# Performance work log

Hardware: AMD Instinct MI355X
Metric: run time of the kernel (lower is better)

The kernel has to match this reference:

```python
import jax, jax.numpy as jnp
import numpy as np

B, F, S = 2, 512, 1024
E = 4
I = 1024          # intermediate = 2 * features
K = 3             # conv kernel size
INIT_SCALE = 1.0
EPS = 1e-5
SLOPE = 0.02


def setup_inputs() -> dict:
    key = jax.random.key(0)
    k = jax.random.split(key, 6)
    inp = jax.random.normal(k[0], (B, F, S), jnp.float32)
    divisor = (jnp.arange(S, dtype=jnp.float32) + 1.0).reshape(1, 1, S)
    w0_gate = jax.random.normal(k[1], (E, F, 1), jnp.float32) * (F ** -0.5)
    w0 = jax.random.normal(k[2], (E, F, 3 * I), jnp.float32) * (F ** -0.5)
    w1 = jax.random.normal(k[3], (3 * I, I, K), jnp.float32) * ((I * K) ** -0.5)
    w2_gate = jax.random.normal(k[4], (E, I, 1), jnp.float32) * (I ** -0.5)
    w2 = jax.random.normal(k[5], (E, I, F), jnp.float32) * (I ** -0.5)
    return {"inp": inp, "divisor": divisor, "w0_gate": w0_gate, "w0": w0,
            "w1": w1, "w2_gate": w2_gate, "w2": w2}


def _norm(x):
    # channel norm over dim 1: subtract mean, divide by scaled L2 norm
    x = x - jnp.mean(x, axis=1, keepdims=True)
    n = jnp.sqrt(jnp.sum(x * x, axis=1, keepdims=True)) * (x.shape[1] ** -0.5)
    return x / (n + EPS)


def _moe(x, gate, w):
    # x: [B,F,S]; gate: [E,F,1]; w: [E,F,D]
    logits = jnp.einsum('bfs,ef->bes', x, gate[:, :, 0])          # [B,E,S]
    gates = jax.nn.softmax(logits, axis=1)
    idx = jnp.argmax(logits, axis=1)                              # [B,S]
    one_hot = jax.nn.one_hot(idx, w.shape[0], dtype=x.dtype)      # [B,S,E]
    # straight-through gumbel-style gate: hard one-hot fwd, soft grad
    gumbel = jnp.transpose(one_hot, (0, 2, 1)) - jax.lax.stop_gradient(gates) + gates  # [B,E,S]
    xs = jnp.transpose(x, (0, 2, 1))                              # [B,S,F]
    out = jnp.zeros((x.shape[0], x.shape[2], w.shape[2]), x.dtype)
    for e in range(w.shape[0]):  # small fixed expert count
        mask = one_hot[:, :, e][:, :, None]                       # [B,S,1]
        out = out + mask * ((xs * gumbel[:, e, :, None]) @ w[e])
    loss = jnp.sum(jnp.mean(gates, axis=(0, 2)) * jnp.mean(one_hot, axis=(0, 1)))
    return loss, jnp.transpose(out, (0, 2, 1))                    # [B,D,S]


def _conv1d(x, w, causal_pad):
    if causal_pad and w.shape[-1] > 1:
        x = jnp.pad(x, ((0, 0), (0, 0), (w.shape[-1] - 1, 0)))
    return jax.lax.conv_general_dilated(
        x, w, window_strides=(1,), padding='VALID',
        dimension_numbers=('NCH', 'OIH', 'NCH'), feature_group_count=1)


def reference(inp, divisor, w0_gate, w0, w1, w2_gate, w2):
    loss0, h = _moe(inp, w0_gate, w0)                 # [B,3I,S]
    depth, scale, shift = jnp.split(h, 3, axis=1)     # each [B,I,S]
    cum = jnp.cumsum(depth, axis=-1)
    h = jax.nn.leaky_relu(_norm(cum / divisor * scale + shift), SLOPE)
    h = _conv1d(h, w1, causal_pad=True)               # [B,3I,S]
    s0, s1, sh = jnp.split(h, 3, axis=1)
    h = jax.nn.leaky_relu(_norm(s0 * s1 + sh), SLOPE)
    loss1, out = _moe(h, w2_gate, w2)                 # [B,F,S]
    return out * INIT_SCALE, loss0 + loss1
```

## Files before the change

### kernel.cpp

```cpp
#include <hip/hip_runtime.h>
#include <hip/hip_bf16.h>

#define SDIM 1024

typedef float f32x4 __attribute__((ext_vector_type(4)));
typedef short short8 __attribute__((ext_vector_type(8)));

__device__ __forceinline__ unsigned short f2bf(float f) {
    __hip_bfloat16 h = __float2bfloat16(f);
    return *reinterpret_cast<unsigned short*>(&h);
}
__device__ __forceinline__ float bf2f(unsigned short u) {
    return __uint_as_float(((unsigned int)u) << 16);
}
__device__ __forceinline__ void gload_lds16(const unsigned short* g, unsigned short* l) {
    __builtin_amdgcn_global_load_lds((const __attribute__((address_space(1))) void*)g,
                                     (__attribute__((address_space(3))) void*)l, 16, 0, 0);
}

__device__ __forceinline__ void tr_split(
    const float* __restrict__ in, unsigned short* __restrict__ oh,
    unsigned short* __restrict__ ol, int R, int C, size_t sliceStride,
    int bx, int by, int slice, int tid, float (*t)[33])
{
    int c0 = bx * 32, r0 = by * 32;
    int cc = tid & 31, r8 = tid >> 5;
    const float* ip = in + slice * sliceStride;
    #pragma unroll
    for (int k = 0; k < 4; ++k) {
        int r = r8 + k * 8;
        t[r][cc] = ip[(size_t)(r0 + r) * C + c0 + cc];
    }
    __syncthreads();
    #pragma unroll
    for (int k = 0; k < 4; ++k) {
        int rr = r8 + k * 8;
        float v = t[cc][rr];
        unsigned short hi = f2bf(v);
        unsigned short lo = f2bf(v - bf2f(hi));
        size_t o = slice * sliceStride + (size_t)(c0 + rr) * R + r0 + cc;
        oh[o] = hi; ol[o] = lo;
    }
}

__global__ __launch_bounds__(256) void prep_kernel(
    const float* __restrict__ inp, const float* __restrict__ w0,
    const float* __restrict__ w1,
    unsigned short* __restrict__ xTh, unsigned short* __restrict__ xTl,
    unsigned short* __restrict__ w0Th, unsigned short* __restrict__ w0Tl,
    unsigned short* __restrict__ w1Th, unsigned short* __restrict__ w1Tl,
    const float* __restrict__ wg, int* __restrict__ idx, float* __restrict__ acc)
{
    __shared__ float t[32][33];
    __shared__ float wgs[4 * 512];
    __shared__ float part[32][4][9];
    __shared__ float la[8];
    int id = blockIdx.x;
    int tid = threadIdx.x;
    if (id < 1024) {
        int bx = id & 31, by = (id >> 5) & 15, slice = id >> 9;
        tr_split(inp, xTh, xTl, 512, 1024, (size_t)512 * 1024, bx, by, slice, tid, t);
    } else if (id < 7168) {
        int m = id - 1024;
        int bx = m % 96, by = (m / 96) & 15, slice = m / 1536;
        tr_split(w0, w0Th, w0Tl, 512, 3072, (size_t)512 * 3072, bx, by, slice, tid, t);
    } else if (id < 19456) {
        int tt = (id - 7168) * 256 + tid;
        int o = tt >> 10, i = tt & 1023;
        const float* p = w1 + (size_t)o * 3072 + i * 3;
        #pragma unroll
        for (int k = 0; k < 3; ++k) {
            float v = p[k];
            unsigned short hi = f2bf(v);
            unsigned short lo = f2bf(v - bf2f(hi));
            size_t off = (size_t)k * 3145728 + (size_t)o * 1024 + i;
            w1Th[off] = hi; w1Tl[off] = lo;
        }
    } else {
        if (tid < 8) la[tid] = 0.f;
        for (int l = tid; l < 2048; l += 256) wgs[l] = wg[l];
        __syncthreads();
        int t0 = (id - 19456) * 8;
        int b = t0 >> 10, s0 = t0 & 1023;
        int sl = tid & 7, fg = tid >> 3;
        float l0 = 0.f, l1 = 0.f, l2 = 0.f, l3 = 0.f;
        for (int f = fg; f < 512; f += 32) {
            float xv = inp[((size_t)b * 512 + f) * SDIM + s0 + sl];
            l0 += xv * wgs[f];
            l1 += xv * wgs[512 + f];
            l2 += xv * wgs[1024 + f];
            l3 += xv * wgs[1536 + f];
        }
        part[fg][0][sl] = l0; part[fg][1][sl] = l1;
        part[fg][2][sl] = l2; part[fg][3][sl] = l3;
        __syncthreads();
        for (int h = 16; h >= 1; h >>= 1) {
            if (fg < h) {
                #pragma unroll
                for (int e = 0; e < 4; ++e) part[fg][e][sl] += part[fg + h][e][sl];
            }
            __syncthreads();
        }
        if (fg == 0) {
            float L[4] = {part[0][0][sl], part[0][1][sl], part[0][2][sl], part[0][3][sl]};
            float m = fmaxf(fmaxf(L[0], L[1]), fmaxf(L[2], L[3]));
            float e0 = expf(L[0] - m), e1 = expf(L[1] - m), e2 = expf(L[2] - m), e3 = expf(L[3] - m);
            float inv = 1.0f / (e0 + e1 + e2 + e3);
            int best = 0; float bv = L[0];
            if (L[1] > bv) { bv = L[1]; best = 1; }
            if (L[2] > bv) { bv = L[2]; best = 2; }
            if (L[3] > bv) { bv = L[3]; best = 3; }
            idx[t0 + sl] = best;
            atomicAdd(&la[0], e0 * inv);
            atomicAdd(&la[1], e1 * inv);
            atomicAdd(&la[2], e2 * inv);
            atomicAdd(&la[3], e3 * inv);
            atomicAdd(&la[4 + best], 1.0f);
        }
        __syncthreads();
        if (tid < 8) atomicAdd(&acc[tid], la[tid]);
    }
}

__global__ __launch_bounds__(1024) void sort_kernel(
    const int* __restrict__ idx, int* __restrict__ perm, int* __restrict__ eSorted)
{
    int b = blockIdx.x;
    int tid = threadIdx.x;
    int lane = tid & 63, w = tid >> 6;
    int e = idx[(b << 10) + tid];
    __shared__ int wcnt[16][4];
    __shared__ int woff[16][4];
    int r = 0;
    unsigned long long lt = (1ull << lane) - 1ull;
    #pragma unroll
    for (int eo = 0; eo < 4; ++eo) {
        unsigned long long m = __ballot(e == eo);
        if (lane == 0) wcnt[w][eo] = __popcll(m);
        if (e == eo) r = __popcll(m & lt);
    }
    __syncthreads();
    if (tid == 0) {
        int baseAcc = 0;
        for (int eo = 0; eo < 4; ++eo)
            for (int ww = 0; ww < 16; ++ww) { woff[ww][eo] = baseAcc; baseAcc += wcnt[ww][eo]; }
    }
    __syncthreads();
    int pos = woff[w][e] + r;
    perm[(b << 10) + pos] = tid;
    eSorted[(b << 10) + pos] = e;
}

__global__ __launch_bounds__(768) void moe_split_kernel(
    const unsigned short* __restrict__ base, unsigned int XH, unsigned int XL,
    unsigned int WH, unsigned int WL,
    const int* __restrict__ perm, const int* __restrict__ eSorted,
    float* __restrict__ out)
{
    extern __shared__ unsigned short lds[];
    const int BUF = 40960;
    int id = blockIdx.x;
    int wg = (id & 7) * 32 + (id >> 3);
    int t0 = (wg & 7) * 256;
    int d0 = (wg >> 3) * 96;
    int b = t0 >> 10, s0 = t0 & 1023;
    int tid = threadIdx.x;
    int lane = tid & 63;
    int lm = lane & 15, q = lane >> 4;
    int wid = tid >> 6;
    int wm = (wid >> 2) * 32, wn = (wid & 3) * 64;

    int eLo = eSorted[(b << 10) + s0];
    int eHi = eSorted[(b << 10) + s0 + 255];

    unsigned int gofs[7];
    int lofs[7], doSeg[7];
    #pragma unroll
    for (int j = 0; j < 7; ++j) {
        int seg = wid + 12 * j;
        gofs[j] = 0; lofs[j] = 0; doSeg[j] = 0;
        if (seg < 80) {
            int row = seg * 16 + (lane >> 2);
            int slot = lane & 3;
            int c = slot ^ ((row >> 1) & 3);
            unsigned int src;
            int act = 1;
            if (row < 512) {
                int gr = (row < 256) ? row : row - 256;
                unsigned int hb = (row < 256) ? XH : XL;
                int tj = perm[(b << 10) + s0 + gr];
                src = hb + (unsigned int)(((b << 10) + tj) * 512) + c * 8;
            } else {
                int R = row - 512;
                unsigned int hb = WH;
                if (R >= 384) { R -= 384; hb = WL; }
                int e = R / 96, dl = R - e * 96;
                act = (e >= eLo && e <= eHi) ? 1 : 0;
                src = hb + (unsigned int)((e * 3072 + d0 + dl) * 512) + c * 8;
            }
            gofs[j] = src;
            lofs[j] = seg * 512 + lane * 8;
            doSeg[j] = act;
        }
    }

    int bofH[4];
    #pragma unroll
    for (int fn = 0; fn < 4; ++fn) {
        int row = wn + fn * 16 + lm;
        bofH[fn] = row * 32 + ((q ^ ((row >> 1) & 3)) << 3);
    }
    int aofH[4][2];
    #pragma unroll
    for (int e = 0; e < 4; ++e)
        #pragma unroll
        for (int fm = 0; fm < 2; ++fm) {
            int row = 512 + e * 96 + wm + fm * 16 + lm;
            aofH[e][fm] = row * 32 + ((q ^ ((row >> 1) & 3)) << 3);
        }

    int eidx[4], sv[4];
    #pragma unroll
    for (int fn = 0; fn < 4; ++fn) {
        int sl = (b << 10) + s0 + wn + fn * 16 + lm;
        eidx[fn] = eSorted[sl];
        sv[fn]   = perm[sl];
    }
    bool presF[4][4], presE[4];
    #pragma unroll
    for (int e = 0; e < 4; ++e) {
        presE[e] = false;
        #pragma unroll
        for (int fn = 0; fn < 4; ++fn) {
            presF[e][fn] = __any(eidx[fn] == e);
            presE[e] = presE[e] || presF[e][fn];
        }
    }

    f32x4 acc[2][4];
    #pragma unroll
    for (int fm = 0; fm < 2; ++fm)
        #pragma unroll
        for (int fn = 0; fn < 4; ++fn)
            acc[fm][fn] = (f32x4){0.f, 0.f, 0.f, 0.f};

    const short8 z = {0, 0, 0, 0, 0, 0, 0, 0};

    #pragma unroll
    for (int j = 0; j < 7; ++j)
        if (doSeg[j]) gload_lds16(base + gofs[j], lds + lofs[j]);

    int curOfs = 0;
    for (int f0 = 0; f0 < 512; f0 += 32) {
        __syncthreads();
        int nxtOfs = curOfs ^ BUF;
        if (f0 + 32 < 512) {
            #pragma unroll
            for (int j = 0; j < 7; ++j)
                if (doSeg[j]) gload_lds16(base + gofs[j] + f0 + 32, lds + nxtOfs + lofs[j]);
        }

        const unsigned short* lb = lds + curOfs;
        short8 bh[4], bl[4];
        #pragma unroll
        for (int fn = 0; fn < 4; ++fn) {
            bh[fn] = *(const short8*)(lb + bofH[fn]);
            bl[fn] = *(const short8*)(lb + bofH[fn] + 8192);
        }
        #pragma unroll
        for (int e = 0; e < 4; ++e) {
            if (presE[e]) {
                short8 ah[2], al[2];
                #pragma unroll
                for (int fm = 0; fm < 2; ++fm) {
                    ah[fm] = *(const short8*)(lb + aofH[e][fm]);
                    al[fm] = *(const short8*)(lb + aofH[e][fm] + 12288);
                }
                __builtin_amdgcn_s_setprio(1);
                #pragma unroll
                for (int fn = 0; fn < 4; ++fn) {
                    if (presF[e][fn]) {
                        short8 bmH = (eidx[fn] == e) ? bh[fn] : z;
                        short8 bmL = (eidx[fn] == e) ? bl[fn] : z;
                        #pragma unroll
                        for (int fm = 0; fm < 2; ++fm) {
                            acc[fm][fn] = __builtin_amdgcn_mfma_f32_16x16x32_bf16(ah[fm], bmH, acc[fm][fn], 0, 0, 0);
                            acc[fm][fn] = __builtin_amdgcn_mfma_f32_16x16x32_bf16(ah[fm], bmL, acc[fm][fn], 0, 0, 0);
                            acc[fm][fn] = __builtin_amdgcn_mfma_f32_16x16x32_bf16(al[fm], bmH, acc[fm][fn], 0, 0, 0);
                        }
                    }
                }
                __builtin_amdgcn_s_setprio(0);
            }
        }
        curOfs = nxtOfs;
    }

    #pragma unroll
    for (int fm = 0; fm < 2; ++fm)
        #pragma unroll
        for (int fn = 0; fn < 4; ++fn) {
            int d = d0 + wm + fm * 16 + q * 4;
            float* op = out + ((size_t)b * 3072 + d) * SDIM + sv[fn];
            #pragma unroll
            for (int r = 0; r < 4; ++r)
                op[(size_t)r * SDIM] = acc[fm][fn][r];
        }
}

__global__ __launch_bounds__(1024) void conv_split_kernel(
    const unsigned short* __restrict__ base, unsigned int GH, unsigned int GL,
    unsigned int WH, unsigned int WL, unsigned int ZB, float* __restrict__ h1T)
{
    extern __shared__ unsigned short lds[];
    const int BUF = 35328;
    int id = blockIdx.x;
    int wg = (id & 7) * 32 + (id >> 3);
    int t0 = (wg & 7) * 256;
    int o0 = (wg >> 3) * 96;
    int b = t0 >> 10, s0 = t0 & 1023;
    int tid = threadIdx.x;
    int lane = tid & 63;
    int lm = lane & 15, q = lane >> 4;
    int wid = tid >> 6;
    int wm = (wid >> 3) * 48, wn = (wid & 7) * 32;
    int krot = wid % 3;

    unsigned int gofs[5];
    int lofs[5];
    int nseg = (wid < 5) ? 5 : 4;
    #pragma unroll
    for (int j = 0; j < 5; ++j) {
        int seg = wid + 16 * j;
        gofs[j] = ZB; lofs[j] = 0;
        if (seg < 69) {
            int row = seg * 16 + (lane >> 2);
            int slot = lane & 3;
            int c = slot ^ ((row >> 1) & 3);
            unsigned int src;
            if (row < 528) {
                int gr = (row < 264) ? row : row - 264;
                unsigned int hb = (row < 264) ? GH : GL;
                int s = s0 - 2 + gr;
                if (s < 0) src = ZB + c * 8;
                else { if (s > 1023) s = 1023;
                       src = hb + ((unsigned int)((b << 10) + s) << 10) + c * 8; }
            } else {
                int R = row - 528;
                unsigned int hb = WH;
                if (R >= 288) { R -= 288; hb = WL; }
                int k = R / 96, ol = R - k * 96;
                src = hb + (unsigned int)k * 3145728u + ((unsigned int)(o0 + ol) << 10) + c * 8;
            }
            gofs[j] = src;
            lofs[j] = seg * 512 + lane * 8;
        }
    }

    int aofH[3][3], aofL[3][3], bofH[3][2], bofL[3][2];
    #pragma unroll
    for (int kk = 0; kk < 3; ++kk) {
        int k = kk + krot; if (k >= 3) k -= 3;
        #pragma unroll
        for (int fm = 0; fm < 3; ++fm) {
            int R = k * 96 + wm + fm * 16 + lm;
            int rh = 528 + R, rl = 816 + R;
            aofH[kk][fm] = rh * 32 + ((q ^ ((rh >> 1) & 3)) << 3);
            aofL[kk][fm] = rl * 32 + ((q ^ ((rl >> 1) & 3)) << 3);
        }
        #pragma unroll
        for (int fn = 0; fn < 2; ++fn) {
            int rh = wn + fn * 16 + lm + k;
            int rl = rh + 264;
            bofH[kk][fn] = rh * 32 + ((q ^ ((rh >> 1) & 3)) << 3);
            bofL[kk][fn] = rl * 32 + ((q ^ ((rl >> 1) & 3)) << 3);
        }
    }

    f32x4 acc[3][2];
    #pragma unroll
    for (int fm = 0; fm < 3; ++fm)
        #pragma unroll
        for (int fn = 0; fn < 2; ++fn)
            acc[fm][fn] = (f32x4){0.f, 0.f, 0.f, 0.f};

    #pragma unroll
    for (int j = 0; j < 5; ++j)
        if (j < nseg) gload_lds16(base + gofs[j], lds + lofs[j]);

    int curOfs = 0;
    for (int i0 = 0; i0 < 1024; i0 += 32) {
        __syncthreads();
        int nxtOfs = curOfs ^ BUF;
        if (i0 + 32 < 1024) {
            #pragma unroll
            for (int j = 0; j < 5; ++j)
                if (j < nseg) gload_lds16(base + gofs[j] + i0 + 32, lds + nxtOfs + lofs[j]);
        }

        const unsigned short* lb = lds + curOfs;
        #pragma unroll
        for (int kk = 0; kk < 3; ++kk) {
            short8 ah[3], al[3], bh[2], bl[2];
            #pragma unroll
            for (int fm = 0; fm < 3; ++fm) {
                ah[fm] = *(const short8*)(lb + aofH[kk][fm]);
                al[fm] = *(const short8*)(lb + aofL[kk][fm]);
            }
            #pragma unroll
            for (int fn = 0; fn < 2; ++fn) {
                bh[fn] = *(const short8*)(lb + bofH[kk][fn]);
                bl[fn] = *(const short8*)(lb + bofL[kk][fn]);
            }
            __builtin_amdgcn_s_setprio(1);
            #pragma unroll
            for (int fm = 0; fm < 3; ++fm)
                #pragma unroll
                for (int fn = 0; fn < 2; ++fn) {
                    acc[fm][fn] = __builtin_amdgcn_mfma_f32_16x16x32_bf16(ah[fm], bh[fn], acc[fm][fn], 0, 0, 0);
                    acc[fm][fn] = __builtin_amdgcn_mfma_f32_16x16x32_bf16(ah[fm], bl[fn], acc[fm][fn], 0, 0, 0);
                    acc[fm][fn] = __builtin_amdgcn_mfma_f32_16x16x32_bf16(al[fm], bh[fn], acc[fm][fn], 0, 0, 0);
                }
            __builtin_amdgcn_s_setprio(0);
        }
        curOfs = nxtOfs;
    }

    #pragma unroll
    for (int fm = 0; fm < 3; ++fm)
        #pragma unroll
        for (int fn = 0; fn < 2; ++fn) {
            int o = o0 + wm + fm * 16 + q * 4;
            int s = s0 + wn + fn * 16 + lm;
            *(f32x4*)(h1T + ((size_t)((b << 10) + s)) * 3072 + o) = acc[fm][fn];
        }
}

__global__ __launch_bounds__(256) void moe_kernel(
    const unsigned short* __restrict__ xT, const unsigned short* __restrict__ wT,
    const int* __restrict__ perm, const int* __restrict__ eSorted,
    float* __restrict__ out, int Fdim, int Ddim, const float* __restrict__ accv)
{
    if (blockIdx.x == 0 && threadIdx.x == 0) {
        float l = 0.f;
        #pragma unroll
        for (int e = 0; e < 4; ++e)
            l += accv[e] * accv[4 + e] + accv[8 + e] * accv[12 + e];
        out[2 * 512 * 1024] = l * (1.0f / (2048.0f * 2048.0f));
    }
    __shared__ unsigned short lds[384 * 32];
    int id = blockIdx.x;
    int chunk = gridDim.x >> 3;
    int wg = (id & 7) * chunk + (id >> 3);
    int t0 = (wg & 15) * 128;
    int d0 = (wg >> 4) * 64;
    int b = t0 >> 10, s0 = t0 & 1023;
    int tid = threadIdx.x;
    int lane = tid & 63, wid = tid >> 6;
    int lm = lane & 15, q = lane >> 4;
    int wm = (wid >> 1) * 32, wn = (wid & 1) * 64;

    int eLo = eSorted[(b << 10) + s0];
    int eHi = eSorted[(b << 10) + s0 + 127];

    const unsigned short* gsrc[6];
    int lofs[6], doSeg[6];
    #pragma unroll
    for (int j = 0; j < 6; ++j) {
        int seg = wid + 4 * j;
        int row = seg * 16 + (lane >> 2);
        int slot = lane & 3;
        int c = slot ^ ((row >> 1) & 3);
        int act = 1;
        const unsigned short* src;
        if (row < 128) {
            int tj = perm[(b << 10) + s0 + row];
            src = xT + (size_t)((b << 10) + tj) * Fdim + c * 8;
        } else {
            int R = row - 128;
            int e = R >> 6;
            act = (e >= eLo && e <= eHi) ? 1 : 0;
            src = wT + (size_t)(e * Ddim + d0 + (R & 63)) * Fdim + c * 8;
        }
        gsrc[j] = src; lofs[j] = seg * 512 + lane * 8; doSeg[j] = act;
    }

    int bof[4], aof[4][2];
    #pragma unroll
    for (int fn = 0; fn < 4; ++fn) {
        int row = wn + fn * 16 + lm;
        bof[fn] = row * 32 + ((q ^ ((row >> 1) & 3)) << 3);
    }
    #pragma unroll
    for (int e = 0; e < 4; ++e)
        #pragma unroll
        for (int fm = 0; fm < 2; ++fm) {
            int R = 128 + e * 64 + wm + fm * 16 + lm;
            aof[e][fm] = R * 32 + ((q ^ ((R >> 1) & 3)) << 3);
        }

    int eidx[4], sv[4];
    #pragma unroll
    for (int fn = 0; fn < 4; ++fn) {
        int sl = (b << 10) + s0 + wn + fn * 16 + lm;
        eidx[fn] = eSorted[sl];
        sv[fn]   = perm[sl];
    }
    bool presF[4][4], presE[4];
    #pragma unroll
    for (int e = 0; e < 4; ++e) {
        presE[e] = false;
        #pragma unroll
        for (int fn = 0; fn < 4; ++fn) {
            presF[e][fn] = __any(eidx[fn] == e);
            presE[e] = presE[e] || presF[e][fn];
        }
    }

    f32x4 acc[2][4];
    #pragma unroll
    for (int fm = 0; fm < 2; ++fm)
        #pragma unroll
        for (int fn = 0; fn < 4; ++fn)
            acc[fm][fn] = (f32x4){0.f, 0.f, 0.f, 0.f};

    const short8 z = {0, 0, 0, 0, 0, 0, 0, 0};

    for (int f0 = 0; f0 < Fdim; f0 += 32) {
        __syncthreads();
        #pragma unroll
        for (int j = 0; j < 6; ++j)
            if (doSeg[j]) gload_lds16(gsrc[j] + f0, lds + lofs[j]);
        __syncthreads();

        short8 bf[4];
        #pragma unroll
        for (int fn = 0; fn < 4; ++fn)
            bf[fn] = *(const short8*)(lds + bof[fn]);
        #pragma unroll
        for (int e = 0; e < 4; ++e) {
            if (presE[e]) {
                short8 af[2];
                #pragma unroll
                for (int fm = 0; fm < 2; ++fm)
                    af[fm] = *(const short8*)(lds + aof[e][fm]);
                #pragma unroll
                for (int fn = 0; fn < 4; ++fn) {
                    if (presF[e][fn]) {
                        short8 bm = (eidx[fn] == e) ? bf[fn] : z;
                        #pragma unroll
                        for (int fm = 0; fm < 2; ++fm)
                            acc[fm][fn] = __builtin_amdgcn_mfma_f32_16x16x32_bf16(af[fm], bm, acc[fm][fn], 0, 0, 0);
                    }
                }
            }
        }
    }

    #pragma unroll
    for (int fm = 0; fm < 2; ++fm)
        #pragma unroll
        for (int fn = 0; fn < 4; ++fn) {
            int d = d0 + wm + fm * 16 + q * 4;
            float* op = out + ((size_t)b * Ddim + d) * SDIM + sv[fn];
            #pragma unroll
            for (int r = 0; r < 4; ++r)
                op[(size_t)r * SDIM] = acc[fm][fn][r];
        }
}

__global__ __launch_bounds__(256) void cumsum_w2t_kernel(
    const float* __restrict__ h1, const float* __restrict__ divisor,
    float* __restrict__ y, const float* __restrict__ w2, unsigned short* __restrict__ w2T)
{
    __shared__ float tsh[32][33];
    __shared__ float wsum[4];
    int blk = blockIdx.x;
    int tid = threadIdx.x;
    if (blk >= 2048) {
        int m = blk - 2048;
        int bx = m & 15, by = (m >> 4) & 31, slice = m >> 9;
        int c0 = bx * 32, r0 = by * 32;
        int cc = tid & 31, r8 = tid >> 5;
        const float* ip = w2 + (size_t)slice * 524288;
        unsigned short* op = w2T + (size_t)slice * 524288;
        #pragma unroll
        for (int k = 0; k < 4; ++k) {
            int r = r8 + k * 8;
            tsh[r][cc] = ip[(size_t)(r0 + r) * 512 + c0 + cc];
        }
        __syncthreads();
        #pragma unroll
        for (int k = 0; k < 4; ++k) {
            int rr = r8 + k * 8;
            op[(size_t)(c0 + rr) * 1024 + r0 + cc] = f2bf(tsh[cc][rr]);
        }
        return;
    }
    int b = blk >> 10, i = blk & 1023;
    const float4* dp = (const float4*)(h1 + ((size_t)b * 3072 + i) * SDIM);
    const float4* sp = (const float4*)(h1 + ((size_t)b * 3072 + 1024 + i) * SDIM);
    const float4* hp = (const float4*)(h1 + ((size_t)b * 3072 + 2048 + i) * SDIM);
    float4 v = dp[tid];
    float c0 = v.x, c1 = c0 + v.y, c2 = c1 + v.z, c3 = c2 + v.w;
    int lane = tid & 63, w = tid >> 6;
    float sc = c3;
    #pragma unroll
    for (int off = 1; off < 64; off <<= 1) {
        float p = __shfl_up(sc, off);
        if (lane >= off) sc += p;
    }
    if (lane == 63) wsum[w] = sc;
    __syncthreads();
    float wbase = 0.f;
    #pragma unroll
    for (int ww = 0; ww < 4; ++ww)
        if (ww < w) wbase += wsum[ww];
    float base = wbase + sc - c3;
    float4 scv = sp[tid], sh = hp[tid];
    float4 dv = ((const float4*)divisor)[tid];
    float4 o;
    o.x = (base + c0) / dv.x * scv.x + sh.x;
    o.y = (base + c1) / dv.y * scv.y + sh.y;
    o.z = (base + c2) / dv.z * scv.z + sh.z;
    o.w = (base + c3) / dv.w * scv.w + sh.w;
    ((float4*)(y + ((size_t)b * 1024 + i) * SDIM))[tid] = o;
}

__global__ __launch_bounds__(256) void norm0_kernel(
    const float* __restrict__ g, unsigned short* __restrict__ oh,
    unsigned short* __restrict__ ol)
{
    int blk = blockIdx.x;
    int b = blk >> 7;
    int s0 = (blk & 127) * 8;
    int tid = threadIdx.x;
    int sg = tid & 7, grp = tid >> 3;
    int s = s0 + sg;
    const float* bp = g + ((size_t)b * 1024) * SDIM + s;
    float v[32];
    float sum = 0.f, ssq = 0.f;
    #pragma unroll
    for (int j = 0; j < 32; ++j) {
        float x = bp[(size_t)(grp * 32 + j) * SDIM];
        v[j] = x; sum += x; ssq += x * x;
    }
    __shared__ float rs[32][8], rq[32][8], stat[2][8];
    rs[grp][sg] = sum; rq[grp][sg] = ssq;
    __syncthreads();
    for (int h = 16; h >= 1; h >>= 1) {
        if (grp < h) { rs[grp][sg] += rs[grp + h][sg]; rq[grp][sg] += rq[grp + h][sg]; }
        __syncthreads();
    }
    if (grp == 0) {
        float S1 = rs[0][sg], S2 = rq[0][sg];
        float mean = S1 * (1.0f / 1024.0f);
        float ssc = fmaxf(S2 - 1024.0f * mean * mean, 0.0f);
        stat[0][sg] = mean;
        stat[1][sg] = 1.0f / (sqrtf(ssc) * (1.0f / 32.0f) + 1e-5f);
    }
    __syncthreads();
    float mean = stat[0][sg], inv = stat[1][sg];
    size_t tbase = (((size_t)b << 10) + s) * 1024 + grp * 32;
    #pragma unroll
    for (int j0 = 0; j0 < 32; j0 += 4) {
        unsigned short uh[4], ul[4];
        #pragma unroll
        for (int jj = 0; jj < 4; ++jj) {
            float o = (v[j0 + jj] - mean) * inv;
            o = (o >= 0.f) ? o : 0.02f * o;
            uh[jj] = f2bf(o);
            ul[jj] = f2bf(o - bf2f(uh[jj]));
        }
        *(ushort4*)(oh + tbase + j0) = (ushort4){uh[0], uh[1], uh[2], uh[3]};
        *(ushort4*)(ol + tbase + j0) = (ushort4){ul[0], ul[1], ul[2], ul[3]};
    }
}

__global__ __launch_bounds__(256) void normgate_kernel(
    const float* __restrict__ h1T, const float* __restrict__ wg,
    unsigned short* __restrict__ outT, int* __restrict__ idx, float* __restrict__ acc)
{
    int blk = blockIdx.x;
    int b = blk >> 7;
    int s0 = (blk & 127) * 8;
    int tid = threadIdx.x;
    int sg = tid & 7, grp = tid >> 3;
    int s = s0 + sg;
    const float* row = h1T + ((size_t)((b << 10) + s)) * 3072;
    float v[32];
    float sum = 0.f, ssq = 0.f;
    #pragma unroll
    for (int j0 = 0; j0 < 32; j0 += 4) {
        int i = grp * 32 + j0;
        float4 av = *(const float4*)(row + i);
        float4 mv = *(const float4*)(row + 1024 + i);
        float4 dv = *(const float4*)(row + 2048 + i);
        float x0 = av.x * mv.x + dv.x;
        float x1 = av.y * mv.y + dv.y;
        float x2 = av.z * mv.z + dv.z;
        float x3 = av.w * mv.w + dv.w;
        v[j0] = x0; v[j0 + 1] = x1; v[j0 + 2] = x2; v[j0 + 3] = x3;
        sum += x0 + x1 + x2 + x3;
        ssq += x0 * x0 + x1 * x1 + x2 * x2 + x3 * x3;
    }
    __shared__ float rs[32][8], rq[32][8], stat[2][8];
    rs[grp][sg] = sum; rq[grp][sg] = ssq;
    __syncthreads();
    for (int h = 16; h >= 1; h >>= 1) {
        if (grp < h) { rs[grp][sg] += rs[grp + h][sg]; rq[grp][sg] += rq[grp + h][sg]; }
        __syncthreads();
    }
    if (grp == 0) {
        float S1 = rs[0][sg], S2 = rq[0][sg];
        float mean = S1 * (1.0f / 1024.0f);
        float ssc = fmaxf(S2 - 1024.0f * mean * mean, 0.0f);
        stat[0][sg] = mean;
        stat[1][sg] = 1.0f / (sqrtf(ssc) * (1.0f / 32.0f) + 1e-5f);
    }
    __syncthreads();
    float mean = stat[0][sg], inv = stat[1][sg];
    float l0 = 0.f, l1 = 0.f, l2 = 0.f, l3 = 0.f;
    size_t tbase = (((size_t)b << 10) + s) * 1024 + grp * 32;
    #pragma unroll
    for (int j0 = 0; j0 < 32; j0 += 4) {
        unsigned short u[4];
        #pragma unroll
        for (int jj = 0; jj < 4; ++jj) {
            int i = grp * 32 + j0 + jj;
            float o = (v[j0 + jj] - mean) * inv;
            o = (o >= 0.f) ? o : 0.02f * o;
            u[jj] = f2bf(o);
            l0 += o * wg[i];
            l1 += o * wg[1024 + i];
            l2 += o * wg[2048 + i];
            l3 += o * wg[3072 + i];
        }
        *(ushort4*)(outT + tbase + j0) = (ushort4){u[0], u[1], u[2], u[3]};
    }
    __shared__ float pl[4][32][8];
    __shared__ float la[8];
    pl[0][grp][sg] = l0; pl[1][grp][sg] = l1;
    pl[2][grp][sg] = l2; pl[3][grp][sg] = l3;
    if (tid < 8) la[tid] = 0.f;
    __syncthreads();
    for (int h = 16; h >= 1; h >>= 1) {
        if (grp < h) {
            #pragma unroll
            for (int e = 0; e < 4; ++e) pl[e][grp][sg] += pl[e][grp + h][sg];
        }
        __syncthreads();
    }
    if (grp == 0) {
        float L[4] = {pl[0][0][sg], pl[1][0][sg], pl[2][0][sg], pl[3][0][sg]};
        float m = fmaxf(fmaxf(L[0], L[1]), fmaxf(L[2], L[3]));
        float e0 = expf(L[0] - m), e1 = expf(L[1] - m), e2 = expf(L[2] - m), e3 = expf(L[3] - m);
        float invs = 1.0f / (e0 + e1 + e2 + e3);
        int best = 0; float bv = L[0];
        if (L[1] > bv) { bv = L[1]; best = 1; }
        if (L[2] > bv) { bv = L[2]; best = 2; }
        if (L[3] > bv) { bv = L[3]; best = 3; }
        idx[(b << 10) + s] = best;
        atomicAdd(&la[0], e0 * invs);
        atomicAdd(&la[1], e1 * invs);
        atomicAdd(&la[2], e2 * invs);
        atomicAdd(&la[3], e3 * invs);
        atomicAdd(&la[4 + best], 1.0f);
    }
    __syncthreads();
    if (tid < 8) atomicAdd(&acc[8 + tid], la[tid]);
}

extern "C" void kernel_launch(void* const* d_in, const int* in_sizes, int n_in,
                              void* d_out, int out_size, void* d_ws, size_t ws_size,
                              hipStream_t stream) {
    const float* inp     = (const float*)d_in[0];
    const float* divisor = (const float*)d_in[1];
    const float* w0_gate = (const float*)d_in[2];
    const float* w0      = (const float*)d_in[3];
    const float* w1      = (const float*)d_in[4];
    const float* w2_gate = (const float*)d_in[5];
    const float* w2      = (const float*)d_in[6];
    float* out = (float*)d_out;
    (void)in_sizes; (void)n_in; (void)out_size; (void)ws_size;

    char* ws = (char*)d_ws;
    const unsigned short* base = (const unsigned short*)ws;

    float* h1            = (float*)(ws + 0);
    float* g             = (float*)(ws + 25165824);
    unsigned short* gT1h = (unsigned short*)(ws + 33554432);
    unsigned short* gT1l = (unsigned short*)(ws + 37748736);
    unsigned short* w1Th = (unsigned short*)(ws + 41943040);
    unsigned short* w1Tl = (unsigned short*)(ws + 60817408);
    unsigned short* xTh  = (unsigned short*)(ws + 79691776);
    unsigned short* xTl  = (unsigned short*)(ws + 81788928);
    unsigned short* w0Th = (unsigned short*)(ws + 83886080);
    unsigned short* w0Tl = (unsigned short*)(ws + 96468992);
    unsigned short* gT2  = (unsigned short*)(ws + 79691776);
    unsigned short* w2T  = (unsigned short*)(ws + 83886080);
    int* idx1            = (int*)(ws + 109051904);
    int* idx2            = (int*)(ws + 109060096);
    float* acc           = (float*)(ws + 109068288);
    int* perm1           = (int*)(ws + 109076480);
    int* eSort1          = (int*)(ws + 109084672);
    int* perm2           = (int*)(ws + 109092864);
    int* eSort2          = (int*)(ws + 109101056);
    float* zbuf          = (float*)(ws + 109109248);

    const unsigned int GT1H = 16777216u, GT1L = 18874368u;
    const unsigned int W1TH = 20971520u, W1TL = 30408704u;
    const unsigned int XTH  = 39845888u, XTL  = 40894464u;
    const unsigned int W0TH = 41943040u, W0TL = 48234496u;
    const unsigned int ZB   = 54554624u;

    hipMemsetAsync(acc, 0, 64, stream);
    hipMemsetAsync(zbuf, 0, 4096, stream);

    prep_kernel<<<19712, 256, 0, stream>>>(inp, w0, w1, xTh, xTl, w0Th, w0Tl,
                                           w1Th, w1Tl, w0_gate, idx1, acc);

    sort_kernel<<<2, 1024, 0, stream>>>(idx1, perm1, eSort1);
    moe_split_kernel<<<256, 768, 163840, stream>>>(base, XTH, XTL, W0TH, W0TL, perm1, eSort1, h1);

    cumsum_w2t_kernel<<<4096, 256, 0, stream>>>(h1, divisor, g, w2, w2T);
    norm0_kernel<<<256, 256, 0, stream>>>(g, gT1h, gT1l);
    conv_split_kernel<<<256, 1024, 141312, stream>>>(base, GT1H, GT1L, W1TH, W1TL, ZB, h1);
    normgate_kernel<<<256, 256, 0, stream>>>(h1, w2_gate, gT2, idx2, acc);

    sort_kernel<<<2, 1024, 0, stream>>>(idx2, perm2, eSort2);
    moe_kernel<<<128, 256, 0, stream>>>(gT2, w2T, perm2, eSort2, out, 1024, 512, acc);
}
```

Measured before the change: 232.7 us.

## Switch conv kernel to 32x32x16 MFMA with 8 waves per block

The conv_split kernel now uses 32x32x16 bf16 MFMA instructions instead of 16x16x32, and each wave computes a 96x32 output tile. The block shrinks from 16 to 8 waves, so each wave issues more global-to-LDS loads per K step. The swizzled LDS offsets, accumulator layout and output store pattern are rewritten to match. The aim is fewer LDS operand reads per flop and better MFMA efficiency, at the cost of less wave-level parallelism to hide latency and more registers per thread.

```diff
diff --git a/kernel.cpp b/kernel.cpp
--- a/kernel.cpp
+++ b/kernel.cpp
@@ -4,6 +4,7 @@
 #define SDIM 1024
 
 typedef float f32x4 __attribute__((ext_vector_type(4)));
+typedef float f32x16 __attribute__((ext_vector_type(16)));
 typedef short short8 __attribute__((ext_vector_type(8)));
 
 __device__ __forceinline__ unsigned short f2bf(float f) {
@@ -308,7 +309,7 @@
         }
 }
 
-__global__ __launch_bounds__(1024) void conv_split_kernel(
+__global__ __launch_bounds__(512) void conv_split_kernel(
     const unsigned short* __restrict__ base, unsigned int GH, unsigned int GL,
     unsigned int WH, unsigned int WL, unsigned int ZB, float* __restrict__ h1T)
 {
@@ -321,17 +322,16 @@
     int b = t0 >> 10, s0 = t0 & 1023;
     int tid = threadIdx.x;
     int lane = tid & 63;
-    int lm = lane & 15, q = lane >> 4;
+    int l32 = lane & 31, half = lane >> 5;
     int wid = tid >> 6;
-    int wm = (wid >> 3) * 48, wn = (wid & 7) * 32;
-    int krot = wid % 3;
-
-    unsigned int gofs[5];
-    int lofs[5];
-    int nseg = (wid < 5) ? 5 : 4;
-    #pragma unroll
-    for (int j = 0; j < 5; ++j) {
-        int seg = wid + 16 * j;
+    int wn = wid * 32;
+
+    unsigned int gofs[9];
+    int lofs[9];
+    int nseg = (wid < 5) ? 9 : 8;
+    #pragma unroll
+    for (int j = 0; j < 9; ++j) {
+        int seg = wid + 8 * j;
         gofs[j] = ZB; lofs[j] = 0;
         if (seg < 69) {
             int row = seg * 16 + (lane >> 2);
@@ -357,35 +357,37 @@
         }
     }
 
-    int aofH[3][3], aofL[3][3], bofH[3][2], bofL[3][2];
+    int aofH[3][3][2], aofL[3][3][2], bofH[3][2], bofL[3][2];
     #pragma unroll
     for (int kk = 0; kk < 3; ++kk) {
-        int k = kk + krot; if (k >= 3) k -= 3;
         #pragma unroll
         for (int fm = 0; fm < 3; ++fm) {
-            int R = k * 96 + wm + fm * 16 + lm;
+            int R = kk * 96 + fm * 32 + l32;
             int rh = 528 + R, rl = 816 + R;
-            aofH[kk][fm] = rh * 32 + ((q ^ ((rh >> 1) & 3)) << 3);
-            aofL[kk][fm] = rl * 32 + ((q ^ ((rl >> 1) & 3)) << 3);
-        }
-        #pragma unroll
-        for (int fn = 0; fn < 2; ++fn) {
-            int rh = wn + fn * 16 + lm + k;
-            int rl = rh + 264;
-            bofH[kk][fn] = rh * 32 + ((q ^ ((rh >> 1) & 3)) << 3);
-            bofL[kk][fn] = rl * 32 + ((q ^ ((rl >> 1) & 3)) << 3);
-        }
-    }
-
-    f32x4 acc[3][2];
+            #pragma unroll
+            for (int ks = 0; ks < 2; ++ks) {
+                aofH[kk][fm][ks] = rh * 32 + (((ks * 2 + half) ^ ((rh >> 1) & 3)) << 3);
+                aofL[kk][fm][ks] = rl * 32 + (((ks * 2 + half) ^ ((rl >> 1) & 3)) << 3);
+            }
+        }
+        int rbh = wn + l32 + kk;
+        int rbl = rbh + 264;
+        #pragma unroll
+        for (int ks = 0; ks < 2; ++ks) {
+            bofH[kk][ks] = rbh * 32 + (((ks * 2 + half) ^ ((rbh >> 1) & 3)) << 3);
+            bofL[kk][ks] = rbl * 32 + (((ks * 2 + half) ^ ((rbl >> 1) & 3)) << 3);
+        }
+    }
+
+    f32x16 acc[3];
     #pragma unroll
     for (int fm = 0; fm < 3; ++fm)
         #pragma unroll
-        for (int fn = 0; fn < 2; ++fn)
-            acc[fm][fn] = (f32x4){0.f, 0.f, 0.f, 0.f};
-
-    #pragma unroll
-    for (int j = 0; j < 5; ++j)
+        for (int j = 0; j < 16; ++j)
+            acc[fm][j] = 0.f;
+
+    #pragma unroll
+    for (int j = 0; j < 9; ++j)
         if (j < nseg) gload_lds16(base + gofs[j], lds + lofs[j]);
 
     int curOfs = 0;
@@ -394,46 +396,46 @@
         int nxtOfs = curOfs ^ BUF;
         if (i0 + 32 < 1024) {
             #pragma unroll
-            for (int j = 0; j < 5; ++j)
+            for (int j = 0; j < 9; ++j)
                 if (j < nseg) gload_lds16(base + gofs[j] + i0 + 32, lds + nxtOfs + lofs[j]);
         }
 
         const unsigned short* lb = lds + curOfs;
         #pragma unroll
-        for (int kk = 0; kk < 3; ++kk) {
-            short8 ah[3], al[3], bh[2], bl[2];
+        for (int ks = 0; ks < 2; ++ks) {
             #pragma unroll
-            for (int fm = 0; fm < 3; ++fm) {
-                ah[fm] = *(const short8*)(lb + aofH[kk][fm]);
-                al[fm] = *(const short8*)(lb + aofL[kk][fm]);
+            for (int kk = 0; kk < 3; ++kk) {
+                short8 bh = *(const short8*)(lb + bofH[kk][ks]);
+                short8 bl = *(const short8*)(lb + bofL[kk][ks]);
+                short8 ah[3], al[3];
+                #pragma unroll
+                for (int fm = 0; fm < 3; ++fm) {
+                    ah[fm] = *(const short8*)(lb + aofH[kk][fm][ks]);
+                    al[fm] = *(const short8*)(lb + aofL[kk][fm][ks]);
+                }
+                __builtin_amdgcn_s_setprio(1);
+                #pragma unroll
+                for (int fm = 0; fm < 3; ++fm) {
+                    acc[fm] = __builtin_amdgcn_mfma_f32_32x32x16_bf16(ah[fm], bh, acc[fm], 0, 0, 0);
+                    acc[fm] = __builtin_amdgcn_mfma_f32_32x32x16_bf16(ah[fm], bl, acc[fm], 0, 0, 0);
+                    acc[fm] = __builtin_amdgcn_mfma_f32_32x32x16_bf16(al[fm], bh, acc[fm], 0, 0, 0);
+                }
+                __builtin_amdgcn_s_setprio(0);
             }
-            #pragma unroll
-            for (int fn = 0; fn < 2; ++fn) {
-                bh[fn] = *(const short8*)(lb + bofH[kk][fn]);
-                bl[fn] = *(const short8*)(lb + bofL[kk][fn]);
-            }
-            __builtin_amdgcn_s_setprio(1);
-            #pragma unroll
-            for (int fm = 0; fm < 3; ++fm)
-                #pragma unroll
-                for (int fn = 0; fn < 2; ++fn) {
-                    acc[fm][fn] = __builtin_amdgcn_mfma_f32_16x16x32_bf16(ah[fm], bh[fn], acc[fm][fn], 0, 0, 0);
-                    acc[fm][fn] = __builtin_amdgcn_mfma_f32_16x16x32_bf16(ah[fm], bl[fn], acc[fm][fn], 0, 0, 0);
-                    acc[fm][fn] = __builtin_amdgcn_mfma_f32_16x16x32_bf16(al[fm], bh[fn], acc[fm][fn], 0, 0, 0);
-                }
-            __builtin_amdgcn_s_setprio(0);
         }
         curOfs = nxtOfs;
     }
 
-    #pragma unroll
-    for (int fm = 0; fm < 3; ++fm)
-        #pragma unroll
-        for (int fn = 0; fn < 2; ++fn) {
-            int o = o0 + wm + fm * 16 + q * 4;
-            int s = s0 + wn + fn * 16 + lm;
-            *(f32x4*)(h1T + ((size_t)((b << 10) + s)) * 3072 + o) = acc[fm][fn];
-        }
+    int s = s0 + wn + l32;
+    float* rowp = h1T + ((size_t)((b << 10) + s)) * 3072 + o0;
+    #pragma unroll
+    for (int fm = 0; fm < 3; ++fm) {
+        #pragma unroll
+        for (int r = 0; r < 4; ++r) {
+            f32x4 v = {acc[fm][4 * r], acc[fm][4 * r + 1], acc[fm][4 * r + 2], acc[fm][4 * r + 3]};
+            *(f32x4*)(rowp + fm * 32 + 8 * r + 4 * half) = v;
+        }
+    }
 }
 
 __global__ __launch_bounds__(256) void moe_kernel(
@@ -825,7 +827,7 @@
 
     cumsum_w2t_kernel<<<4096, 256, 0, stream>>>(h1, divisor, g, w2, w2T);
     norm0_kernel<<<256, 256, 0, stream>>>(g, gT1h, gT1l);
-    conv_split_kernel<<<256, 1024, 141312, stream>>>(base, GT1H, GT1L, W1TH, W1TL, ZB, h1);
+    conv_split_kernel<<<256, 512, 141312, stream>>>(base, GT1H, GT1L, W1TH, W1TL, ZB, h1);
     normgate_kernel<<<256, 256, 0, stream>>>(h1, w2_gate, gT2, idx2, acc);
 
     sort_kernel<<<2, 1024, 0, stream>>>(idx2, perm2, eSort2);
```

New measurement: 250.4 us. 1.08x slower.
